# Optimization experiments

Hardware: AMD Instinct MI355X
Metric: run time of the kernel (lower is better)

Reference implementation:

```python
import jax, jax.numpy as jnp
import numpy as np

HIDDEN = 1024
NUM_HEADS = 16
HEAD_DIM = HIDDEN // NUM_HEADS  # 64
B, S = 4, 1024


def setup_inputs() -> dict:
    key = jax.random.key(0)
    ks = jax.random.split(key, 8)
    xavier = jax.nn.initializers.xavier_uniform()
    inputs = jax.random.normal(ks[0], (B, S, HIDDEN), dtype=jnp.float32)
    context = jax.random.normal(ks[1], (B, S, HIDDEN), dtype=jnp.float32)
    # multiplicative mask: 1 = attend, 0 = ignore (causal), broadcast over batch/heads
    mask = jnp.tril(jnp.ones((S, S), dtype=jnp.float32))[None, None, :, :]
    Wq = xavier(ks[2], (HIDDEN, HIDDEN), jnp.float32)
    bq = jnp.zeros((HIDDEN,), jnp.float32)
    Wk = xavier(ks[3], (HIDDEN, HEAD_DIM), jnp.float32)
    bk = jnp.zeros((HEAD_DIM,), jnp.float32)
    Wv = xavier(ks[4], (HIDDEN, HEAD_DIM), jnp.float32)
    bv = jnp.zeros((HEAD_DIM,), jnp.float32)
    Wo = xavier(ks[5], (HIDDEN, HIDDEN), jnp.float32)
    bo = jnp.zeros((HIDDEN,), jnp.float32)
    return {"inputs": inputs, "context": context, "mask": mask,
            "Wq": Wq, "bq": bq, "Wk": Wk, "bk": bk,
            "Wv": Wv, "bv": bv, "Wo": Wo, "bo": bo}


def reference(inputs, context, mask, Wq, bq, Wk, bk, Wv, bv, Wo, bo):
    query = inputs @ Wq + bq                      # (B, S, D)
    key = context @ Wk + bk                       # (B, S, D/H)
    value = context @ Wv + bv                     # (B, S, D/H)
    # MQA: broadcast single KV head to all query heads via interleaved repeat
    key = jnp.repeat(key, NUM_HEADS, axis=-1)     # (B, S, D)
    value = jnp.repeat(value, NUM_HEADS, axis=-1) # (B, S, D)
    bsz = query.shape[0]
    Lq, Lk = query.shape[1], key.shape[1]
    # faithful to original: plain reshape (not transpose) into heads
    qh = jnp.reshape(query, (bsz, NUM_HEADS, Lq, HEAD_DIM))
    kh = jnp.reshape(key, (bsz, NUM_HEADS, Lk, HEAD_DIM))
    vh = jnp.reshape(value, (bsz, NUM_HEADS, Lk, HEAD_DIM))
    # note: original scales by sqrt(key.shape[-1]) == sqrt(hidden_dim)
    scores = jnp.einsum('bhqd,bhkd->bhqk', qh, kh) / jnp.sqrt(jnp.float32(HIDDEN))
    scores = scores * mask                        # multiplicative mask
    attn = jax.nn.softmax(scores, axis=-1)        # (B, H, Lq, Lk)
    ctx = jnp.einsum('bhqk,bhkd->bhqd', attn, vh)
    ctx = jnp.reshape(ctx, (bsz, Lq, HIDDEN))
    outputs = ctx @ Wo + bo                       # (B, S, D)
    return outputs, attn
```

## Files before the change

kernel.cpp:

```cpp
#include <hip/hip_runtime.h>
#include <hip/hip_bf16.h>
#include <cstdint>

#define NHEADS 16
#define SEQ    1024
#define BATCH  4

typedef float vfloat4 __attribute__((ext_vector_type(4)));

__device__ __forceinline__ float wave_max(float v){
  #pragma unroll
  for (int off = 32; off > 0; off >>= 1) v = fmaxf(v, __shfl_xor(v, off));
  return v;
}
__device__ __forceinline__ float wave_sum(float v){
  #pragma unroll
  for (int off = 32; off > 0; off >>= 1) v += __shfl_xor(v, off);
  return v;
}
__device__ __forceinline__ void nt_store4(float* p, float x, float y, float z, float w){
  vfloat4 v; v.x = x; v.y = y; v.z = z; v.w = w;
  __builtin_nontemporal_store(v, (vfloat4*)p);
}

__global__ __launch_bounds__(256) void prep_kernel(
    const float* __restrict__ Wq, const float* __restrict__ bq,
    const float* __restrict__ Wo,
    float* __restrict__ WqSum, float* __restrict__ bqSum, float* __restrict__ WoSum)
{
  const int blk = blockIdx.x, tid = threadIdx.x;
  if (blk < 256){
    const int c = blk * 4 + (tid >> 6), g = tid & 63;
    const float* p = &Wq[(size_t)c * 1024 + (g << 4)];
    float s = 0.f;
    #pragma unroll
    for (int f = 0; f < 16; ++f) s += p[f];
    WqSum[c * 64 + g] = s;
  } else if (blk < 320){
    const int g = blk - 256;
    for (int m = tid; m < 1024; m += 256){
      float s = 0.f;
      #pragma unroll
      for (int f = 0; f < 16; ++f) s += Wo[(size_t)((g << 4) + f) * 1024 + m];
      WoSum[g * 1024 + m] = s;
    }
  } else {
    if (tid < 64){
      float s = 0.f;
      #pragma unroll
      for (int f = 0; f < 16; ++f) s += bq[(tid << 4) + f];
      bqSum[tid] = s;
    }
  }
}

__global__ __launch_bounds__(256) void qkv_split(
    const float* __restrict__ inputs, const float* __restrict__ context,
    const float* __restrict__ WqSum,
    const float* __restrict__ Wk, const float* __restrict__ Wv,
    float* __restrict__ part)
{
  __shared__ float As[2][16][68];
  __shared__ float Bs[2][16][68];
  const int z = blockIdx.y, sz = blockIdx.z;
  const float* A = (z == 0) ? inputs : context;
  const float* B = (z == 0) ? WqSum : ((z == 1) ? Wk : Wv);
  const int m0 = blockIdx.x * 64;
  const int ks = sz << 8;
  const int tid = threadIdx.x;
  const int tx = tid & 15, ty = tid >> 4;
  const int arow = tid >> 2, acg = (tid & 3) << 2;
  const int brow = tid >> 4, bcg = (tid & 15) << 2;

  float4 av  = *(const float4*)&A[(size_t)(m0 + arow) * 1024 + ks + acg];
  float4 bvv = *(const float4*)&B[(size_t)(ks + brow) * 64 + bcg];
  As[0][acg + 0][arow] = av.x; As[0][acg + 1][arow] = av.y;
  As[0][acg + 2][arow] = av.z; As[0][acg + 3][arow] = av.w;
  *(float4*)&Bs[0][brow][bcg] = bvv;
  __syncthreads();

  float acc[4][4] = {};
  for (int t = 0; t < 16; ++t){
    const int cur = t & 1;
    if (t < 15){
      const int k0 = ks + ((t + 1) << 4);
      av  = *(const float4*)&A[(size_t)(m0 + arow) * 1024 + k0 + acg];
      bvv = *(const float4*)&B[(size_t)(k0 + brow) * 64 + bcg];
    }
    #pragma unroll
    for (int kk = 0; kk < 16; ++kk){
      const float4 a  = *(const float4*)&As[cur][kk][ty << 2];
      const float4 bb = *(const float4*)&Bs[cur][kk][tx << 2];
      const float a_[4] = {a.x, a.y, a.z, a.w};
      const float b_[4] = {bb.x, bb.y, bb.z, bb.w};
      #pragma unroll
      for (int i = 0; i < 4; ++i)
        #pragma unroll
        for (int j = 0; j < 4; ++j) acc[i][j] += a_[i] * b_[j];
    }
    if (t < 15){
      As[cur ^ 1][acg + 0][arow] = av.x; As[cur ^ 1][acg + 1][arow] = av.y;
      As[cur ^ 1][acg + 2][arow] = av.z; As[cur ^ 1][acg + 3][arow] = av.w;
      *(float4*)&Bs[cur ^ 1][brow][bcg] = bvv;
    }
    __syncthreads();
  }
  float* P = part + ((size_t)(z * 4 + sz) * 4096 + m0) * 64;
  #pragma unroll
  for (int i = 0; i < 4; ++i)
    *(float4*)&P[(size_t)((ty << 2) + i) * 64 + (tx << 2)] =
      make_float4(acc[i][0], acc[i][1], acc[i][2], acc[i][3]);
}

__global__ __launch_bounds__(256) void attn_fused(
    const float* __restrict__ part,
    const float* __restrict__ bqSum, const float* __restrict__ bk,
    const float* __restrict__ bv,
    const float* __restrict__ WoSum, const float* __restrict__ bo,
    float* __restrict__ outp, float* __restrict__ attnp)
{
  __shared__ float BmT[4][1032];
  __shared__ float VmT[4][1032];
  __shared__ float Aq[64][4];
  __shared__ float bsum16[16];
  __shared__ float SufT[4][5];
  __shared__ float CtxS[4][64];

  const int tid = threadIdx.x;
  const int qb = blockIdx.x;
  const int h  = blockIdx.y;
  const int b  = blockIdx.z;
  const int base = b * SEQ + h * 64;

  for (int idx = tid; idx < 4096; idx += 256){
    const int r = idx >> 6, c = idx & 63;
    const size_t off = (size_t)(base + r) * 64 + c;
    float kacc = bk[c], vacc = bv[c];
    #pragma unroll
    for (int s = 0; s < 4; ++s){
      kacc += part[(size_t)(4 + s) * 262144 + off];
      vacc += part[(size_t)(8 + s) * 262144 + off];
    }
    const int k = (r << 4) + (c >> 2), e = c & 3;
    BmT[e][k] = kacc;
    VmT[e][k] = vacc;
  }
  {
    const int p_l = tid >> 6, g = tid & 63;
    float qacc = bqSum[g];
    const size_t off = (size_t)(base + (qb << 2) + p_l) * 64 + g;
    #pragma unroll
    for (int s = 0; s < 4; ++s) qacc += part[(size_t)s * 262144 + off];
    Aq[(p_l << 4) + (g >> 2)][g & 3] = qacc;
  }
  __syncthreads();
  {
    const int pair = tid >> 4, sub = tid & 15;
    const int e = pair >> 2, jj = pair & 3;
    float s = 0.f;
    #pragma unroll
    for (int n = 0; n < 16; ++n) s += VmT[e][(jj << 8) + (n << 4) + sub];
    #pragma unroll
    for (int off2 = 8; off2 > 0; off2 >>= 1) s += __shfl_xor(s, off2);
    if (sub == 0) bsum16[pair] = s;
  }
  __syncthreads();
  if (tid < 4){
    float s = 0.f;
    SufT[tid][4] = 0.f;
    for (int jj = 3; jj >= 0; --jj){ s += bsum16[tid * 4 + jj]; SufT[tid][jj] = s; }
  }
  __syncthreads();

  const int wave = tid >> 6, lane = tid & 63;
  for (int i = 0; i < 16; ++i){
    const int ql = (wave << 4) + i;
    const int q  = (qb << 6) + ql;
    const float4 a = *(const float4*)&Aq[ql][0];
    const int jdot = (q >> 8) + 1;
    float4 sv[4];
    float mloc = (q == 1023) ? -3.0e38f : 0.0f;
    #pragma unroll
    for (int j = 0; j < 4; ++j){
      if (j < jdot){
        const int k0 = (lane << 2) + (j << 8);
        const float4 b0 = *(const float4*)&BmT[0][k0];
        const float4 b1 = *(const float4*)&BmT[1][k0];
        const float4 b2 = *(const float4*)&BmT[2][k0];
        const float4 b3 = *(const float4*)&BmT[3][k0];
        float4 t;
        t.x = (a.x*b0.x + a.y*b1.x + a.z*b2.x + a.w*b3.x) * 0.03125f;
        t.y = (a.x*b0.y + a.y*b1.y + a.z*b2.y + a.w*b3.y) * 0.03125f;
        t.z = (a.x*b0.z + a.y*b1.z + a.z*b2.z + a.w*b3.z) * 0.03125f;
        t.w = (a.x*b0.w + a.y*b1.w + a.z*b2.w + a.w*b3.w) * 0.03125f;
        t.x = (k0     <= q) ? t.x : 0.0f;
        t.y = (k0 + 1 <= q) ? t.y : 0.0f;
        t.z = (k0 + 2 <= q) ? t.z : 0.0f;
        t.w = (k0 + 3 <= q) ? t.w : 0.0f;
        sv[j] = t;
        mloc = fmaxf(mloc, fmaxf(fmaxf(t.x, t.y), fmaxf(t.z, t.w)));
      }
    }
    const float m  = wave_max(mloc);
    const float em = __expf(-m);
    float Zl = 0.f, c0 = 0.f, c1 = 0.f, c2 = 0.f, c3 = 0.f;
    #pragma unroll
    for (int j = 0; j < 4; ++j){
      if (j < jdot){
        const int k0 = (lane << 2) + (j << 8);
        const float e0 = __expf(sv[j].x - m);
        const float e1 = __expf(sv[j].y - m);
        const float e2 = __expf(sv[j].z - m);
        const float e3 = __expf(sv[j].w - m);
        Zl += (e0 + e1) + (e2 + e3);
        const float4 v0 = *(const float4*)&VmT[0][k0];
        const float4 v1 = *(const float4*)&VmT[1][k0];
        const float4 v2 = *(const float4*)&VmT[2][k0];
        const float4 v3 = *(const float4*)&VmT[3][k0];
        c0 += e0*v0.x + e1*v0.y + e2*v0.z + e3*v0.w;
        c1 += e0*v1.x + e1*v1.y + e2*v1.z + e3*v1.w;
        c2 += e0*v2.x + e1*v2.y + e2*v2.z + e3*v2.w;
        c3 += e0*v3.x + e1*v3.y + e2*v3.z + e3*v3.w;
        sv[j] = make_float4(e0, e1, e2, e3);
      }
    }
    const int ktail = jdot << 8;
    const float Z = wave_sum(Zl) + em * (float)(1024 - ktail);
    c0 = wave_sum(c0) + em * SufT[0][jdot];
    c1 = wave_sum(c1) + em * SufT[1][jdot];
    c2 = wave_sum(c2) + em * SufT[2][jdot];
    c3 = wave_sum(c3) + em * SufT[3][jdot];
    const float invZ = 1.0f / Z;

    float* rowp = attnp + (((size_t)(b * NHEADS + h) << 10) + (size_t)q) * 1024;
    #pragma unroll
    for (int j = 0; j < 4; ++j){
      if (j < jdot){
        const int k0 = (lane << 2) + (j << 8);
        nt_store4(rowp + k0, sv[j].x * invZ, sv[j].y * invZ,
                             sv[j].z * invZ, sv[j].w * invZ);
      }
    }
    const float fv = em * invZ;
    for (int rr = 0; rr < 4 - jdot; ++rr){
      nt_store4(rowp + ktail + (rr << 8) + (lane << 2), fv, fv, fv, fv);
    }
    if (lane == 0){
      *(float4*)&CtxS[wave][i << 2] =
        make_float4(c0 * invZ, c1 * invZ, c2 * invZ, c3 * invZ);
    }
  }
  __syncthreads();

  {
    const int i = tid >> 6, t = tid & 63;
    float4 acc[4];
    #pragma unroll
    for (int jj = 0; jj < 4; ++jj) acc[jj] = make_float4(0.f, 0.f, 0.f, 0.f);
    for (int g = 0; g < 64; ++g){
      const float cg = CtxS[i][g];
      const float* wrow = &WoSum[(size_t)g * 1024 + (t << 2)];
      #pragma unroll
      for (int jj = 0; jj < 4; ++jj){
        const float4 w = *(const float4*)&wrow[jj << 8];
        acc[jj].x += cg * w.x; acc[jj].y += cg * w.y;
        acc[jj].z += cg * w.z; acc[jj].w += cg * w.w;
      }
    }
    const size_t R = (size_t)(base + (qb << 2) + i);
    #pragma unroll
    for (int jj = 0; jj < 4; ++jj){
      const float4 bov = *(const float4*)&bo[(jj << 8) + (t << 2)];
      nt_store4(&outp[R * 1024 + (jj << 8) + (t << 2)],
                acc[jj].x + bov.x, acc[jj].y + bov.y,
                acc[jj].z + bov.z, acc[jj].w + bov.w);
    }
  }
}

extern "C" void kernel_launch(void* const* d_in, const int* in_sizes, int n_in,
                              void* d_out, int out_size, void* d_ws, size_t ws_size,
                              hipStream_t stream)
{
  const float* inputs  = (const float*)d_in[0];
  const float* context = (const float*)d_in[1];
  const float* Wq = (const float*)d_in[3];
  const float* bq = (const float*)d_in[4];
  const float* Wk = (const float*)d_in[5];
  const float* bk = (const float*)d_in[6];
  const float* Wv = (const float*)d_in[7];
  const float* bv = (const float*)d_in[8];
  const float* Wo = (const float*)d_in[9];
  const float* bo = (const float*)d_in[10];

  float* outp  = (float*)d_out;
  float* attnp = outp + (size_t)BATCH * SEQ * 1024;

  float* ws    = (float*)d_ws;
  float* WqSum = ws;
  float* bqSum = ws + 65536;
  float* WoSum = ws + 65600;
  float* part  = ws + 131136;

  prep_kernel<<<dim3(321), dim3(256), 0, stream>>>(Wq, bq, Wo, WqSum, bqSum, WoSum);
  qkv_split <<<dim3(64, 3, 4), dim3(256), 0, stream>>>(inputs, context, WqSum,
                                                       Wk, Wv, part);
  attn_fused<<<dim3(16, 16, 4), dim3(256), 0, stream>>>(part, bqSum, bk, bv,
                                                        WoSum, bo, outp, attnp);
}
```

Before: 128.2 us.

## Keep K/V tiles in registers instead of LDS and compute suffix sums per wave

Each lane now loads its slice of the reduced K and V partial sums straight into registers with float4 global loads, replacing the transposed LDS tiles. The suffix sums of V used for the masked tail are computed per block with wave reductions, since jdot is the same for every query in a block, which removes two barriers and the LDS reduction stages. This drops about 33KB of LDS per block, which may allow more blocks per CU, but adds 128 VGPRs of K/V state per thread, which could raise register pressure or cause spills.

```diff
diff --git a/kernel.cpp b/kernel.cpp
--- a/kernel.cpp
+++ b/kernel.cpp
@@ -119,11 +119,7 @@
     const float* __restrict__ WoSum, const float* __restrict__ bo,
     float* __restrict__ outp, float* __restrict__ attnp)
 {
-  __shared__ float BmT[4][1032];
-  __shared__ float VmT[4][1032];
   __shared__ float Aq[64][4];
-  __shared__ float bsum16[16];
-  __shared__ float SufT[4][5];
   __shared__ float CtxS[4][64];
 
   const int tid = threadIdx.x;
@@ -131,68 +127,72 @@
   const int h  = blockIdx.y;
   const int b  = blockIdx.z;
   const int base = b * SEQ + h * 64;
-
-  for (int idx = tid; idx < 4096; idx += 256){
-    const int r = idx >> 6, c = idx & 63;
-    const size_t off = (size_t)(base + r) * 64 + c;
-    float kacc = bk[c], vacc = bv[c];
-    #pragma unroll
-    for (int s = 0; s < 4; ++s){
-      kacc += part[(size_t)(4 + s) * 262144 + off];
-      vacc += part[(size_t)(8 + s) * 262144 + off];
-    }
-    const int k = (r << 4) + (c >> 2), e = c & 3;
-    BmT[e][k] = kacc;
-    VmT[e][k] = vacc;
-  }
+  const int wave = tid >> 6, lane = tid & 63;
+
   {
-    const int p_l = tid >> 6, g = tid & 63;
+    const int g = lane;
     float qacc = bqSum[g];
-    const size_t off = (size_t)(base + (qb << 2) + p_l) * 64 + g;
+    const size_t off = (size_t)(base + (qb << 2) + wave) * 64 + g;
     #pragma unroll
     for (int s = 0; s < 4; ++s) qacc += part[(size_t)s * 262144 + off];
-    Aq[(p_l << 4) + (g >> 2)][g & 3] = qacc;
+    Aq[(wave << 4) + (g >> 2)][g & 3] = qacc;
   }
   __syncthreads();
-  {
-    const int pair = tid >> 4, sub = tid & 15;
-    const int e = pair >> 2, jj = pair & 3;
-    float s = 0.f;
-    #pragma unroll
-    for (int n = 0; n < 16; ++n) s += VmT[e][(jj << 8) + (n << 4) + sub];
-    #pragma unroll
-    for (int off2 = 8; off2 > 0; off2 >>= 1) s += __shfl_xor(s, off2);
-    if (sub == 0) bsum16[pair] = s;
-  }
-  __syncthreads();
-  if (tid < 4){
-    float s = 0.f;
-    SufT[tid][4] = 0.f;
-    for (int jj = 3; jj >= 0; --jj){ s += bsum16[tid * 4 + jj]; SufT[tid][jj] = s; }
-  }
-  __syncthreads();
-
-  const int wave = tid >> 6, lane = tid & 63;
+
+  const int krow = lane >> 2;
+  const int kcol = (lane & 3) << 4;
+  float4 Kreg[4][4], Vreg[4][4];
+  #pragma unroll
+  for (int j = 0; j < 4; ++j){
+    const size_t roff = (size_t)(base + krow + (j << 4)) * 64 + kcol;
+    #pragma unroll
+    for (int d = 0; d < 4; ++d){
+      float4 ka = *(const float4*)&bk[kcol + (d << 2)];
+      float4 va = *(const float4*)&bv[kcol + (d << 2)];
+      #pragma unroll
+      for (int s = 0; s < 4; ++s){
+        const float4 kp = *(const float4*)&part[(size_t)(4 + s) * 262144 + roff + (d << 2)];
+        ka.x += kp.x; ka.y += kp.y; ka.z += kp.z; ka.w += kp.w;
+      }
+      #pragma unroll
+      for (int s = 0; s < 4; ++s){
+        const float4 vp = *(const float4*)&part[(size_t)(8 + s) * 262144 + roff + (d << 2)];
+        va.x += vp.x; va.y += vp.y; va.z += vp.z; va.w += vp.w;
+      }
+      Kreg[j][d] = ka; Vreg[j][d] = va;
+    }
+  }
+
+  const int jdot  = (qb >> 2) + 1;
+  const int ktail = jdot << 8;
+  float s0 = 0.f, s1 = 0.f, s2 = 0.f, s3 = 0.f;
+  #pragma unroll
+  for (int jj = 0; jj < 4; ++jj){
+    if (jj >= jdot){
+      s0 += Vreg[jj][0].x + Vreg[jj][1].x + Vreg[jj][2].x + Vreg[jj][3].x;
+      s1 += Vreg[jj][0].y + Vreg[jj][1].y + Vreg[jj][2].y + Vreg[jj][3].y;
+      s2 += Vreg[jj][0].z + Vreg[jj][1].z + Vreg[jj][2].z + Vreg[jj][3].z;
+      s3 += Vreg[jj][0].w + Vreg[jj][1].w + Vreg[jj][2].w + Vreg[jj][3].w;
+    }
+  }
+  const float suf0 = wave_sum(s0), suf1 = wave_sum(s1);
+  const float suf2 = wave_sum(s2), suf3 = wave_sum(s3);
+
   for (int i = 0; i < 16; ++i){
     const int ql = (wave << 4) + i;
     const int q  = (qb << 6) + ql;
     const float4 a = *(const float4*)&Aq[ql][0];
-    const int jdot = (q >> 8) + 1;
     float4 sv[4];
     float mloc = (q == 1023) ? -3.0e38f : 0.0f;
     #pragma unroll
     for (int j = 0; j < 4; ++j){
       if (j < jdot){
         const int k0 = (lane << 2) + (j << 8);
-        const float4 b0 = *(const float4*)&BmT[0][k0];
-        const float4 b1 = *(const float4*)&BmT[1][k0];
-        const float4 b2 = *(const float4*)&BmT[2][k0];
-        const float4 b3 = *(const float4*)&BmT[3][k0];
         float4 t;
-        t.x = (a.x*b0.x + a.y*b1.x + a.z*b2.x + a.w*b3.x) * 0.03125f;
-        t.y = (a.x*b0.y + a.y*b1.y + a.z*b2.y + a.w*b3.y) * 0.03125f;
-        t.z = (a.x*b0.z + a.y*b1.z + a.z*b2.z + a.w*b3.z) * 0.03125f;
-        t.w = (a.x*b0.w + a.y*b1.w + a.z*b2.w + a.w*b3.w) * 0.03125f;
+        t.x = (a.x*Kreg[j][0].x + a.y*Kreg[j][0].y + a.z*Kreg[j][0].z + a.w*Kreg[j][0].w) * 0.03125f;
+        t.y = (a.x*Kreg[j][1].x + a.y*Kreg[j][1].y + a.z*Kreg[j][1].z + a.w*Kreg[j][1].w) * 0.03125f;
+        t.z = (a.x*Kreg[j][2].x + a.y*Kreg[j][2].y + a.z*Kreg[j][2].z + a.w*Kreg[j][2].w) * 0.03125f;
+        t.w = (a.x*Kreg[j][3].x + a.y*Kreg[j][3].y + a.z*Kreg[j][3].z + a.w*Kreg[j][3].w) * 0.03125f;
         t.x = (k0     <= q) ? t.x : 0.0f;
         t.y = (k0 + 1 <= q) ? t.y : 0.0f;
         t.z = (k0 + 2 <= q) ? t.z : 0.0f;
@@ -207,29 +207,23 @@
     #pragma unroll
     for (int j = 0; j < 4; ++j){
       if (j < jdot){
-        const int k0 = (lane << 2) + (j << 8);
         const float e0 = __expf(sv[j].x - m);
         const float e1 = __expf(sv[j].y - m);
         const float e2 = __expf(sv[j].z - m);
         const float e3 = __expf(sv[j].w - m);
         Zl += (e0 + e1) + (e2 + e3);
-        const float4 v0 = *(const float4*)&VmT[0][k0];
-        const float4 v1 = *(const float4*)&VmT[1][k0];
-        const float4 v2 = *(const float4*)&VmT[2][k0];
-        const float4 v3 = *(const float4*)&VmT[3][k0];
-        c0 += e0*v0.x + e1*v0.y + e2*v0.z + e3*v0.w;
-        c1 += e0*v1.x + e1*v1.y + e2*v1.z + e3*v1.w;
-        c2 += e0*v2.x + e1*v2.y + e2*v2.z + e3*v2.w;
-        c3 += e0*v3.x + e1*v3.y + e2*v3.z + e3*v3.w;
+        c0 += e0*Vreg[j][0].x + e1*Vreg[j][1].x + e2*Vreg[j][2].x + e3*Vreg[j][3].x;
+        c1 += e0*Vreg[j][0].y + e1*Vreg[j][1].y + e2*Vreg[j][2].y + e3*Vreg[j][3].y;
+        c2 += e0*Vreg[j][0].z + e1*Vreg[j][1].z + e2*Vreg[j][2].z + e3*Vreg[j][3].z;
+        c3 += e0*Vreg[j][0].w + e1*Vreg[j][1].w + e2*Vreg[j][2].w + e3*Vreg[j][3].w;
         sv[j] = make_float4(e0, e1, e2, e3);
       }
     }
-    const int ktail = jdot << 8;
     const float Z = wave_sum(Zl) + em * (float)(1024 - ktail);
-    c0 = wave_sum(c0) + em * SufT[0][jdot];
-    c1 = wave_sum(c1) + em * SufT[1][jdot];
-    c2 = wave_sum(c2) + em * SufT[2][jdot];
-    c3 = wave_sum(c3) + em * SufT[3][jdot];
+    c0 = wave_sum(c0) + em * suf0;
+    c1 = wave_sum(c1) + em * suf1;
+    c2 = wave_sum(c2) + em * suf2;
+    c3 = wave_sum(c3) + em * suf3;
     const float invZ = 1.0f / Z;
 
     float* rowp = attnp + (((size_t)(b * NHEADS + h) << 10) + (size_t)q) * 1024;
```

Result: slower. 207.0 us (+61.5%).

## Drop softmax max pass and process two query rows per iteration

Applied to the files above, without the earlier changes.

Removes the row-max reduction and max-subtraction from the softmax, exponentiating raw scaled scores directly. Masked positions, which are zero, now contribute exp(0)=1 to the normalizer. The loop now handles two query rows per iteration so each K/V shared-memory load is reused twice, and the tail-block count and suffix sums are hoisted out of the loop. This saves a wave reduction and extra exp work per row, at the cost of possible overflow if scores grow large and higher register pressure.

```diff
diff --git a/kernel.cpp b/kernel.cpp
--- a/kernel.cpp
+++ b/kernel.cpp
@@ -8,11 +8,6 @@
 
 typedef float vfloat4 __attribute__((ext_vector_type(4)));
 
-__device__ __forceinline__ float wave_max(float v){
-  #pragma unroll
-  for (int off = 32; off > 0; off >>= 1) v = fmaxf(v, __shfl_xor(v, off));
-  return v;
-}
 __device__ __forceinline__ float wave_sum(float v){
   #pragma unroll
   for (int off = 32; off > 0; off >>= 1) v += __shfl_xor(v, off);
@@ -173,13 +168,20 @@
   __syncthreads();
 
   const int wave = tid >> 6, lane = tid & 63;
-  for (int i = 0; i < 16; ++i){
-    const int ql = (wave << 4) + i;
-    const int q  = (qb << 6) + ql;
-    const float4 a = *(const float4*)&Aq[ql][0];
-    const int jdot = (q >> 8) + 1;
-    float4 sv[4];
-    float mloc = (q == 1023) ? -3.0e38f : 0.0f;
+  const int jdot  = (qb >> 2) + 1;
+  const int ktail = jdot << 8;
+  const float ztail = (float)(1024 - ktail);
+  const float suf0 = SufT[0][jdot], suf1 = SufT[1][jdot];
+  const float suf2 = SufT[2][jdot], suf3 = SufT[3][jdot];
+
+  for (int i = 0; i < 16; i += 2){
+    const int qlA = (wave << 4) + i;
+    const int qA  = (qb << 6) + qlA, qB = qA + 1;
+    const float4 aA = *(const float4*)&Aq[qlA][0];
+    const float4 aB = *(const float4*)&Aq[qlA + 1][0];
+    float4 svA[4], svB[4];
+    float ZA = 0.f, ZB = 0.f;
+    float cA0=0.f,cA1=0.f,cA2=0.f,cA3=0.f, cB0=0.f,cB1=0.f,cB2=0.f,cB3=0.f;
     #pragma unroll
     for (int j = 0; j < 4; ++j){
       if (j < jdot){
@@ -188,66 +190,75 @@
         const float4 b1 = *(const float4*)&BmT[1][k0];
         const float4 b2 = *(const float4*)&BmT[2][k0];
         const float4 b3 = *(const float4*)&BmT[3][k0];
-        float4 t;
-        t.x = (a.x*b0.x + a.y*b1.x + a.z*b2.x + a.w*b3.x) * 0.03125f;
-        t.y = (a.x*b0.y + a.y*b1.y + a.z*b2.y + a.w*b3.y) * 0.03125f;
-        t.z = (a.x*b0.z + a.y*b1.z + a.z*b2.z + a.w*b3.z) * 0.03125f;
-        t.w = (a.x*b0.w + a.y*b1.w + a.z*b2.w + a.w*b3.w) * 0.03125f;
-        t.x = (k0     <= q) ? t.x : 0.0f;
-        t.y = (k0 + 1 <= q) ? t.y : 0.0f;
-        t.z = (k0 + 2 <= q) ? t.z : 0.0f;
-        t.w = (k0 + 3 <= q) ? t.w : 0.0f;
-        sv[j] = t;
-        mloc = fmaxf(mloc, fmaxf(fmaxf(t.x, t.y), fmaxf(t.z, t.w)));
-      }
-    }
-    const float m  = wave_max(mloc);
-    const float em = __expf(-m);
-    float Zl = 0.f, c0 = 0.f, c1 = 0.f, c2 = 0.f, c3 = 0.f;
-    #pragma unroll
-    for (int j = 0; j < 4; ++j){
-      if (j < jdot){
-        const int k0 = (lane << 2) + (j << 8);
-        const float e0 = __expf(sv[j].x - m);
-        const float e1 = __expf(sv[j].y - m);
-        const float e2 = __expf(sv[j].z - m);
-        const float e3 = __expf(sv[j].w - m);
-        Zl += (e0 + e1) + (e2 + e3);
+        float4 tA, tB;
+        tA.x = (aA.x*b0.x + aA.y*b1.x + aA.z*b2.x + aA.w*b3.x) * 0.03125f;
+        tA.y = (aA.x*b0.y + aA.y*b1.y + aA.z*b2.y + aA.w*b3.y) * 0.03125f;
+        tA.z = (aA.x*b0.z + aA.y*b1.z + aA.z*b2.z + aA.w*b3.z) * 0.03125f;
+        tA.w = (aA.x*b0.w + aA.y*b1.w + aA.z*b2.w + aA.w*b3.w) * 0.03125f;
+        tB.x = (aB.x*b0.x + aB.y*b1.x + aB.z*b2.x + aB.w*b3.x) * 0.03125f;
+        tB.y = (aB.x*b0.y + aB.y*b1.y + aB.z*b2.y + aB.w*b3.y) * 0.03125f;
+        tB.z = (aB.x*b0.z + aB.y*b1.z + aB.z*b2.z + aB.w*b3.z) * 0.03125f;
+        tB.w = (aB.x*b0.w + aB.y*b1.w + aB.z*b2.w + aB.w*b3.w) * 0.03125f;
+        tA.x = (k0     <= qA) ? tA.x : 0.0f;
+        tA.y = (k0 + 1 <= qA) ? tA.y : 0.0f;
+        tA.z = (k0 + 2 <= qA) ? tA.z : 0.0f;
+        tA.w = (k0 + 3 <= qA) ? tA.w : 0.0f;
+        tB.x = (k0     <= qB) ? tB.x : 0.0f;
+        tB.y = (k0 + 1 <= qB) ? tB.y : 0.0f;
+        tB.z = (k0 + 2 <= qB) ? tB.z : 0.0f;
+        tB.w = (k0 + 3 <= qB) ? tB.w : 0.0f;
+        const float eA0 = __expf(tA.x), eA1 = __expf(tA.y);
+        const float eA2 = __expf(tA.z), eA3 = __expf(tA.w);
+        const float eB0 = __expf(tB.x), eB1 = __expf(tB.y);
+        const float eB2 = __expf(tB.z), eB3 = __expf(tB.w);
+        ZA += (eA0 + eA1) + (eA2 + eA3);
+        ZB += (eB0 + eB1) + (eB2 + eB3);
         const float4 v0 = *(const float4*)&VmT[0][k0];
         const float4 v1 = *(const float4*)&VmT[1][k0];
         const float4 v2 = *(const float4*)&VmT[2][k0];
         const float4 v3 = *(const float4*)&VmT[3][k0];
-        c0 += e0*v0.x + e1*v0.y + e2*v0.z + e3*v0.w;
-        c1 += e0*v1.x + e1*v1.y + e2*v1.z + e3*v1.w;
-        c2 += e0*v2.x + e1*v2.y + e2*v2.z + e3*v2.w;
-        c3 += e0*v3.x + e1*v3.y + e2*v3.z + e3*v3.w;
-        sv[j] = make_float4(e0, e1, e2, e3);
+        cA0 += eA0*v0.x + eA1*v0.y + eA2*v0.z + eA3*v0.w;
+        cA1 += eA0*v1.x + eA1*v1.y + eA2*v1.z + eA3*v1.w;
+        cA2 += eA0*v2.x + eA1*v2.y + eA2*v2.z + eA3*v2.w;
+        cA3 += eA0*v3.x + eA1*v3.y + eA2*v3.z + eA3*v3.w;
+        cB0 += eB0*v0.x + eB1*v0.y + eB2*v0.z + eB3*v0.w;
+        cB1 += eB0*v1.x + eB1*v1.y + eB2*v1.z + eB3*v1.w;
+        cB2 += eB0*v2.x + eB1*v2.y + eB2*v2.z + eB3*v2.w;
+        cB3 += eB0*v3.x + eB1*v3.y + eB2*v3.z + eB3*v3.w;
+        svA[j] = make_float4(eA0, eA1, eA2, eA3);
+        svB[j] = make_float4(eB0, eB1, eB2, eB3);
       }
     }
-    const int ktail = jdot << 8;
-    const float Z = wave_sum(Zl) + em * (float)(1024 - ktail);
-    c0 = wave_sum(c0) + em * SufT[0][jdot];
-    c1 = wave_sum(c1) + em * SufT[1][jdot];
-    c2 = wave_sum(c2) + em * SufT[2][jdot];
-    c3 = wave_sum(c3) + em * SufT[3][jdot];
-    const float invZ = 1.0f / Z;
-
-    float* rowp = attnp + (((size_t)(b * NHEADS + h) << 10) + (size_t)q) * 1024;
+    const float ZAt = wave_sum(ZA) + ztail;
+    const float ZBt = wave_sum(ZB) + ztail;
+    cA0 = wave_sum(cA0) + suf0; cA1 = wave_sum(cA1) + suf1;
+    cA2 = wave_sum(cA2) + suf2; cA3 = wave_sum(cA3) + suf3;
+    cB0 = wave_sum(cB0) + suf0; cB1 = wave_sum(cB1) + suf1;
+    cB2 = wave_sum(cB2) + suf2; cB3 = wave_sum(cB3) + suf3;
+    const float invZA = 1.0f / ZAt, invZB = 1.0f / ZBt;
+
+    float* rowA = attnp + (((size_t)(b * NHEADS + h) << 10) + (size_t)qA) * 1024;
+    float* rowB = rowA + 1024;
     #pragma unroll
     for (int j = 0; j < 4; ++j){
       if (j < jdot){
         const int k0 = (lane << 2) + (j << 8);
-        nt_store4(rowp + k0, sv[j].x * invZ, sv[j].y * invZ,
-                             sv[j].z * invZ, sv[j].w * invZ);
+        nt_store4(rowA + k0, svA[j].x * invZA, svA[j].y * invZA,
+                             svA[j].z * invZA, svA[j].w * invZA);
+        nt_store4(rowB + k0, svB[j].x * invZB, svB[j].y * invZB,
+                             svB[j].z * invZB, svB[j].w * invZB);
       }
     }
-    const float fv = em * invZ;
     for (int rr = 0; rr < 4 - jdot; ++rr){
-      nt_store4(rowp + ktail + (rr << 8) + (lane << 2), fv, fv, fv, fv);
+      const int kf = ktail + (rr << 8) + (lane << 2);
+      nt_store4(rowA + kf, invZA, invZA, invZA, invZA);
+      nt_store4(rowB + kf, invZB, invZB, invZB, invZB);
     }
     if (lane == 0){
       *(float4*)&CtxS[wave][i << 2] =
-        make_float4(c0 * invZ, c1 * invZ, c2 * invZ, c3 * invZ);
+        make_float4(cA0 * invZA, cA1 * invZA, cA2 * invZA, cA3 * invZA);
+      *(float4*)&CtxS[wave][(i + 1) << 2] =
+        make_float4(cB0 * invZB, cB1 * invZB, cB2 * invZB, cB3 * invZB);
     }
   }
   __syncthreads();
```

After: 124.1 us. 3.2% less time.
